# Performance work log

Measured on AMD Instinct MI355X. Metric: run time of the kernel, lower is better.

Reference implementation:

```python
import jax, jax.numpy as jnp
import numpy as np

B, S, D = 2, 2048, 1024
H = 16
HD = D // H  # 64

def setup_inputs() -> dict:
    key = jax.random.key(0)
    ks = jax.random.split(key, 6)
    scale = 0.02
    x   = jax.random.normal(ks[0], (B, S, D), dtype=jnp.float32)
    Wq  = jax.random.normal(ks[1], (D, D), dtype=jnp.float32) * scale
    Wk  = jax.random.normal(ks[2], (D, D), dtype=jnp.float32) * scale
    Wv  = jax.random.normal(ks[3], (D, D), dtype=jnp.float32) * scale
    Wo  = jax.random.normal(ks[4], (D, D), dtype=jnp.float32) * scale
    bo  = jax.random.normal(ks[5], (D,), dtype=jnp.float32) * scale
    return {"x": x, "Wq": Wq, "Wk": Wk, "Wv": Wv, "Wo": Wo, "bo": bo}

def reference(x, Wq, Wk, Wv, Wo, bo):
    b, s, d = x.shape
    # QKV projections (no bias, qkv_bias=False); weights stored as [d_in, d_out]
    q = (x @ Wq).reshape(b, s, H, HD).transpose(0, 2, 1, 3)  # [b,h,s,hd]
    k = (x @ Wk).reshape(b, s, H, HD).transpose(0, 2, 1, 3)
    v = (x @ Wv).reshape(b, s, H, HD).transpose(0, 2, 1, 3)
    scores = jnp.einsum('bhqd,bhkd->bhqk', q, k)  # [b,h,s,s]
    causal = jnp.triu(jnp.ones((s, s), dtype=bool), k=1)
    scores = jnp.where(causal, -jnp.inf, scores)
    attn = jax.nn.softmax(scores / jnp.sqrt(jnp.float32(HD)), axis=-1)
    # dropout_rate = 0.0 -> identity
    ctx = jnp.einsum('bhqk,bhkd->bqhd', attn, v).reshape(b, s, d)
    return ctx @ Wo + bo
```

## Files before the change

kernel.cpp:

```cpp
#include <hip/hip_runtime.h>
#include <hip/hip_bf16.h>
#include <math.h>

#define B_ 2
#define S_ 2048
#define D_ 1024
#define H_ 16
#define HD_ 64
#define M_ (B_*S_)

typedef __attribute__((ext_vector_type(8))) short bf16x8;
typedef __attribute__((ext_vector_type(4))) float f32x4;

#define MFMA16(a,b,c) __builtin_amdgcn_mfma_f32_16x16x32_bf16(a,b,c,0,0,0)
#define INFF __builtin_inff()

static __device__ __forceinline__ unsigned short f2bf_bits(float f) {
    unsigned int u = __float_as_uint(f);
    unsigned int r = (u + 0x7fffu + ((u >> 16) & 1u)) >> 16;
    return (unsigned short)r;
}

static __device__ __forceinline__ void gload16(const unsigned short* g, unsigned short* l) {
    __builtin_amdgcn_global_load_lds(
        (const __attribute__((address_space(1))) unsigned int*)(g),
        (__attribute__((address_space(3))) unsigned int*)(l),
        16, 0, 0);
}

#define PH_END4 do { \
    asm volatile("s_waitcnt vmcnt(4)" ::: "memory"); \
    __builtin_amdgcn_sched_barrier(0); \
    __builtin_amdgcn_s_barrier(); \
    __builtin_amdgcn_sched_barrier(0); \
} while (0)
#define PH_END6 do { \
    asm volatile("s_waitcnt vmcnt(6)" ::: "memory"); \
    __builtin_amdgcn_sched_barrier(0); \
    __builtin_amdgcn_s_barrier(); \
    __builtin_amdgcn_sched_barrier(0); \
} while (0)

__global__ __launch_bounds__(256) void convert_x_kernel(
    const float* __restrict__ x, unsigned short* __restrict__ o) {
    size_t i = (size_t)blockIdx.x * 256 + threadIdx.x;
    float4 v = reinterpret_cast<const float4*>(x)[i];
    ushort4 u;
    u.x = f2bf_bits(v.x); u.y = f2bf_bits(v.y);
    u.z = f2bf_bits(v.z); u.w = f2bf_bits(v.w);
    reinterpret_cast<ushort4*>(o)[i] = u;
}

__global__ __launch_bounds__(256) void convw_kernel(
    const float* __restrict__ W0, const float* __restrict__ W1,
    const float* __restrict__ W2, const float* __restrict__ W3,
    unsigned short* __restrict__ OT) {
    __shared__ float t[32][33];
    const float* W = (blockIdx.z == 0) ? W0 : (blockIdx.z == 1) ? W1
                    : (blockIdx.z == 2) ? W2 : W3;
    unsigned short* O = OT + (size_t)blockIdx.z * D_ * D_;
    int tx = threadIdx.x & 31, ty = threadIdx.x >> 5;
    int kb = blockIdx.y * 32, nb = blockIdx.x * 32;
#pragma unroll
    for (int i = 0; i < 4; i++)
        t[ty + 8*i][tx] = W[(size_t)(kb + ty + 8*i) * D_ + nb + tx];
    __syncthreads();
#pragma unroll
    for (int i = 0; i < 4; i++) {
        int n = nb + ty + 8*i, k = kb + tx;
        O[(size_t)n * D_ + k] = f2bf_bits(t[tx][ty + 8*i]);
    }
}

__global__ __launch_bounds__(512, 2) void gemm_qkv256(
    const unsigned short* __restrict__ A,
    const unsigned short* __restrict__ BT,
    unsigned short* __restrict__ outp)
{
    __shared__ union {
        struct { unsigned short A[2][2][8192]; unsigned short B[2][2][8192]; } s;
        unsigned short vt[256][136];
    } sm;
    const int tid = threadIdx.x, lane = tid & 63, wid = tid >> 6;
    const int lrow = lane & 15, lk8 = lane >> 4, orow = lk8 * 4;
    const int wmo = (wid >> 2) * 64;
    const int wno = (wid & 3) * 32;
    const int m0 = blockIdx.x * 256, n0 = blockIdx.y * 256;

    const int srow = lane >> 3, sgr = lane & 7;
    const unsigned sgo = (unsigned)(wid * 8 + srow) * 1024u
                       + (unsigned)((sgr ^ srow) << 3);
    const unsigned short* Ag = A  + (unsigned)m0 * 1024u + sgo;
    const unsigned short* Bg = BT + (unsigned)n0 * 1024u + sgo;
    const int ldsrb = wid * 512;

    const int sw0 = ((lk8 ^ (lrow & 7)) << 3);
    const int sw1 = (((4 | lk8) ^ (lrow & 7)) << 3);
    int ar[4], br[2];
#pragma unroll
    for (int f = 0; f < 4; f++) ar[f] = (wmo + f * 16 + lrow) * 64;
#pragma unroll
    for (int g = 0; g < 2; g++) br[g] = (wno + g * 16 + lrow) * 64;

    f32x4 acc[8][4] = {};
    bf16x8 af[4][2], bf[2][2];

    auto stA = [&](int par, int mh, unsigned k) {
        unsigned short* d = &sm.s.A[par][mh][ldsrb];
        const unsigned short* g = Ag + (unsigned)mh * 131072u + k;
        gload16(g, d);
        gload16(g + 65536u, d + 4096);
    };
    auto stB = [&](int par, int nh, unsigned k) {
        unsigned short* d = &sm.s.B[par][nh][ldsrb];
        const unsigned short* g = Bg + (unsigned)nh * 131072u + k;
        gload16(g, d);
        gload16(g + 65536u, d + 4096);
    };
    auto lda = [&](int par, int qm) {
        const unsigned short* p = &sm.s.A[par][qm][0];
#pragma unroll
        for (int f = 0; f < 4; f++) {
            af[f][0] = *reinterpret_cast<const bf16x8*>(p + ar[f] + sw0);
            af[f][1] = *reinterpret_cast<const bf16x8*>(p + ar[f] + sw1);
        }
    };
    auto ldb = [&](int par, int qn) {
        const unsigned short* p = &sm.s.B[par][qn][0];
#pragma unroll
        for (int g = 0; g < 2; g++) {
            bf[g][0] = *reinterpret_cast<const bf16x8*>(p + br[g] + sw0);
            bf[g][1] = *reinterpret_cast<const bf16x8*>(p + br[g] + sw1);
        }
    };
    auto mma = [&](int qm, int qn) {
        __builtin_amdgcn_s_setprio(1);
#pragma unroll
        for (int f = 0; f < 4; f++)
#pragma unroll
            for (int g = 0; g < 2; g++)
#pragma unroll
                for (int ks = 0; ks < 2; ks++)
                    acc[qm*4+f][qn*2+g] =
                        MFMA16(af[f][ks], bf[g][ks], acc[qm*4+f][qn*2+g]);
        __builtin_amdgcn_s_setprio(0);
    };

    stB(0, 0, 0); stA(0, 0, 0); stB(0, 1, 0); stA(0, 1, 0);
    PH_END4;

#pragma unroll 1
    for (int t = 0; t < 16; t++) {
        const int par = t & 1, pn = par ^ 1;
        const unsigned kn = (t < 15) ? (unsigned)(t + 1) * 64u : 0u;
        lda(par, 0); ldb(par, 0);  stB(pn, 0, kn);  mma(0, 0);  PH_END4;
        ldb(par, 1);               stA(pn, 0, kn);  mma(0, 1);  PH_END4;
        lda(par, 1);               stB(pn, 1, kn);  mma(1, 1);  PH_END6;
        ldb(par, 0);               stA(pn, 1, kn);  mma(1, 0);  PH_END4;
    }

    asm volatile("s_waitcnt vmcnt(0)" ::: "memory");
    __builtin_amdgcn_sched_barrier(0);
    __builtin_amdgcn_s_barrier();

    const int which = n0 >> 10;
    const int nl0 = n0 & 1023;
    const int bq = m0 >> 11;
    unsigned short* obase = outp + (size_t)which * 4194304;

    if (which < 2) {
        const float scale = (which == 0) ? 0.125f : 1.0f;
#pragma unroll
        for (int fi = 0; fi < 8; fi++)
#pragma unroll
            for (int g = 0; g < 4; g++)
#pragma unroll
                for (int r = 0; r < 4; r++) {
                    int m = m0 + (fi >> 2) * 128 + wmo + (fi & 3) * 16 + orow + r;
                    int n = nl0 + (g >> 1) * 128 + wno + (g & 1) * 16 + lrow;
                    int s = m & 2047;
                    obase[(((size_t)(bq * 16 + (n >> 6)) * 2048 + s) << 6) + (n & 63)]
                        = f2bf_bits(acc[fi][g][r] * scale);
                }
    } else {
#pragma unroll
        for (int qm = 0; qm < 2; qm++) {
#pragma unroll
            for (int f = 0; f < 4; f++)
#pragma unroll
                for (int g = 0; g < 4; g++) {
                    const int ml = wmo + f * 16 + orow;
                    const int nc = (g >> 1) * 128 + wno + (g & 1) * 16 + lrow;
                    uint2 w;
                    w.x = (unsigned)f2bf_bits(acc[qm*4+f][g][0])
                        | ((unsigned)f2bf_bits(acc[qm*4+f][g][1]) << 16);
                    w.y = (unsigned)f2bf_bits(acc[qm*4+f][g][2])
                        | ((unsigned)f2bf_bits(acc[qm*4+f][g][3]) << 16);
                    *reinterpret_cast<uint2*>(&sm.vt[nc][ml]) = w;
                }
            __syncthreads();
            {
                const int row = tid >> 1, c0 = (tid & 1) * 64;
                unsigned short* dst = obase +
                    ((size_t)(bq * 1024) + nl0 + row) * 2048 +
                    (m0 & 2047) + qm * 128 + c0;
#pragma unroll
                for (int j = 0; j < 64; j += 8)
                    *reinterpret_cast<bf16x8*>(dst + j) =
                        *reinterpret_cast<const bf16x8*>(&sm.vt[row][c0 + j]);
            }
            __syncthreads();
        }
    }
}

template<int BN, int MODE>
__global__ __launch_bounds__(256) void gemm_gl(
    const unsigned short* __restrict__ A,
    const unsigned short* __restrict__ BT,
    void* __restrict__ outp,
    const float* __restrict__ bias)
{
    constexpr int K = 1024;
    constexpr int NF = (BN == 128) ? 4 : 2;
    __shared__ struct { unsigned short As[128][64]; unsigned short Bs[BN][64]; } sm;
    const int m0 = blockIdx.x * 128;
    const int n0 = blockIdx.y * BN;
    const int tid = threadIdx.x, lane = tid & 63, wid = tid >> 6;
    const int wm = (wid >> 1) * 64;
    const int wn = (wid & 1) * (BN / 2);
    const int lrow = lane & 15, lk8 = lane >> 4, orow = lk8 * 4;
    f32x4 acc[4][NF] = {};

    for (int k0 = 0; k0 < K; k0 += 64) {
#pragma unroll
        for (int i = 0; i < 4; i++) {
            const int rbase = wid * 32 + i * 8;
            const int rl = rbase + (lane >> 3);
            const int sc = ((lane & 7) ^ (rl & 7)) << 3;
            gload16(A + (size_t)(m0 + rl) * K + k0 + sc, &sm.As[rbase][0]);
        }
#pragma unroll
        for (int i = 0; i < BN / 32; i++) {
            const int rbase = wid * (BN / 4) + i * 8;
            const int rl = rbase + (lane >> 3);
            const int sc = ((lane & 7) ^ (rl & 7)) << 3;
            gload16(BT + (size_t)(n0 + rl) * K + k0 + sc, &sm.Bs[rbase][0]);
        }
        __syncthreads();
#pragma unroll
        for (int ks = 0; ks < 2; ks++) {
            bf16x8 af[4], bfr[NF];
#pragma unroll
            for (int f = 0; f < 4; f++) {
                const int row = wm + f * 16 + lrow;
                const int p = (ks * 4 + lk8) ^ (row & 7);
                af[f] = *reinterpret_cast<const bf16x8*>(&sm.As[row][p * 8]);
            }
#pragma unroll
            for (int f = 0; f < NF; f++) {
                const int row = wn + f * 16 + lrow;
                const int p = (ks * 4 + lk8) ^ (row & 7);
                bfr[f] = *reinterpret_cast<const bf16x8*>(&sm.Bs[row][p * 8]);
            }
            __builtin_amdgcn_s_setprio(1);
#pragma unroll
            for (int mf = 0; mf < 4; mf++)
#pragma unroll
                for (int nf = 0; nf < NF; nf++)
                    acc[mf][nf] = MFMA16(af[mf], bfr[nf], acc[mf][nf]);
            __builtin_amdgcn_s_setprio(0);
        }
        __syncthreads();
    }

    float* o = (float*)outp;
#pragma unroll
    for (int mf = 0; mf < 4; mf++)
#pragma unroll
        for (int nf = 0; nf < NF; nf++)
#pragma unroll
            for (int r = 0; r < 4; r++) {
                int m = m0 + wm + mf*16 + orow + r;
                int n = n0 + wn + nf*16 + lrow;
                o[(size_t)m * 1024 + n] = acc[mf][nf][r] + bias[n];
            }
}

__global__ __launch_bounds__(256) void attn_kernel(
    const unsigned short* __restrict__ Q,
    const unsigned short* __restrict__ Kb,
    const unsigned short* __restrict__ VT,
    unsigned short* __restrict__ ctx)
{
    __shared__ unsigned short Ks[2][64][64];
    __shared__ unsigned short Vs[2][64][64];
    __shared__ unsigned short Pl[4][16][72];
    const int fid = blockIdx.x;
    const int xcd = fid & 7, t = fid >> 3;
    const int bh = xcd | ((t & 3) << 3);
    const int qt = 31 - (t >> 2);
    const int lane = threadIdx.x & 63, wid = threadIdx.x >> 6;
    const int lrow = lane & 15, lk8 = lane >> 4, orow = lk8 * 4;
    const unsigned short* Qp = Q  + (size_t)bh * (S_ * 64);
    const unsigned short* Kp = Kb + (size_t)bh * (S_ * 64);
    const unsigned short* Vp = VT + (size_t)bh * (64 * S_);
    const int b = bh >> 4, h = bh & 15;
    const int q0 = qt * 64 + wid * 16;
    const int nb = qt + 1;

    auto stage = [&](int buf, int kv0) {
#pragma unroll
        for (int i = 0; i < 2; i++) {
            const int rbase = wid * 16 + 8 * i;
            const int rl = rbase + (lane >> 3);
            const int sc = (((lane & 7) ^ (rl & 7)) << 3);
            gload16(Kp + (size_t)(kv0 + rl) * 64 + sc, &Ks[buf][rbase][0]);
            gload16(Vp + (size_t)rl * S_ + kv0 + sc, &Vs[buf][rbase][0]);
        }
    };

    stage(0, 0);

    bf16x8 qf[2];
#pragma unroll
    for (int kt = 0; kt < 2; kt++)
        qf[kt] = *reinterpret_cast<const bf16x8*>(
            Qp + (size_t)(q0 + lrow) * 64 + kt*32 + lk8*8);

    f32x4 acc[4] = {};
    float lr = 0.f;

    __syncthreads();

#pragma unroll 1
    for (int kvb = 0; kvb < nb; kvb++) {
        const int cur = kvb & 1;
        if (kvb + 1 < nb) stage(cur ^ 1, (kvb + 1) * 64);

        f32x4 sacc[4] = {};
        __builtin_amdgcn_s_setprio(1);
#pragma unroll
        for (int kt = 0; kt < 2; kt++)
#pragma unroll
            for (int nf = 0; nf < 4; nf++) {
                const int row = nf * 16 + lrow;
                const int g = ((kt << 2) | lk8) ^ (row & 7);
                bf16x8 kf = *reinterpret_cast<const bf16x8*>(&Ks[cur][row][g << 3]);
                sacc[nf] = MFMA16(kf, qf[kt], sacc[nf]);
            }
        __builtin_amdgcn_s_setprio(0);
        if (kvb == qt) {
#pragma unroll
            for (int nf = 0; nf < 4; nf++)
#pragma unroll
                for (int r = 0; r < 4; r++)
                    if (nf*16 + orow + r > wid*16 + lrow) sacc[nf][r] = -INFF;
        }
#pragma unroll
        for (int nf = 0; nf < 4; nf++)
#pragma unroll
            for (int r = 0; r < 4; r++) {
                float p = __expf(sacc[nf][r]);
                sacc[nf][r] = p;
                lr += p;
            }
#pragma unroll
        for (int nf = 0; nf < 4; nf++) {
            uint2 w;
            w.x = (unsigned)f2bf_bits(sacc[nf][0]) | ((unsigned)f2bf_bits(sacc[nf][1]) << 16);
            w.y = (unsigned)f2bf_bits(sacc[nf][2]) | ((unsigned)f2bf_bits(sacc[nf][3]) << 16);
            *reinterpret_cast<uint2*>(&Pl[wid][lrow][nf*16 + orow]) = w;
        }
        bf16x8 pf[2];
#pragma unroll
        for (int kt = 0; kt < 2; kt++)
            pf[kt] = *reinterpret_cast<const bf16x8*>(&Pl[wid][lrow][kt*32 + lk8*8]);
        __builtin_amdgcn_s_setprio(1);
#pragma unroll
        for (int kt = 0; kt < 2; kt++)
#pragma unroll
            for (int nf = 0; nf < 4; nf++) {
                const int row = nf * 16 + lrow;
                const int g = ((kt << 2) | lk8) ^ (row & 7);
                bf16x8 vf = *reinterpret_cast<const bf16x8*>(&Vs[cur][row][g << 3]);
                acc[nf] = MFMA16(pf[kt], vf, acc[nf]);
            }
        __builtin_amdgcn_s_setprio(0);
        __syncthreads();
    }

    lr += __shfl_xor(lr, 16);
    lr += __shfl_xor(lr, 32);
    const float inv = 1.0f / lr;
#pragma unroll
    for (int r = 0; r < 4; r++) {
        const float linv = __shfl(inv, (lane & 48) + orow + r);
#pragma unroll
        for (int nf = 0; nf < 4; nf++) {
            int s = q0 + orow + r;
            int col = h * 64 + nf * 16 + lrow;
            ctx[((size_t)(b * S_ + s)) * D_ + col] = f2bf_bits(acc[nf][r] * linv);
        }
    }
}

extern "C" void kernel_launch(void* const* d_in, const int* in_sizes, int n_in,
                              void* d_out, int out_size, void* d_ws, size_t ws_size,
                              hipStream_t stream) {
    const float* x  = (const float*)d_in[0];
    const float* Wq = (const float*)d_in[1];
    const float* Wk = (const float*)d_in[2];
    const float* Wv = (const float*)d_in[3];
    const float* Wo = (const float*)d_in[4];
    const float* bo = (const float*)d_in[5];
    float* out = (float*)d_out;

    char* ws = (char*)d_ws;
    unsigned short* xb  = (unsigned short*)(ws);
    unsigned short* WT  = (unsigned short*)(ws + 8388608);
    unsigned short* QKV = (unsigned short*)(ws + 16777216);
    unsigned short* ctx = (unsigned short*)(ws + 41943040);

    unsigned short* Qb  = QKV;
    unsigned short* Kb  = QKV + 4194304;
    unsigned short* VTb = QKV + 8388608;

    convert_x_kernel<<<dim3(4096), dim3(256), 0, stream>>>(x, xb);
    convw_kernel<<<dim3(32, 32, 4), dim3(256), 0, stream>>>(Wq, Wk, Wv, Wo, WT);

    gemm_qkv256<<<dim3(16, 12), dim3(512), 0, stream>>>(xb, WT, QKV);

    attn_kernel<<<dim3(1024), dim3(256), 0, stream>>>(Qb, Kb, VTb, ctx);

    gemm_gl<64, 1><<<dim3(32, 16), dim3(256), 0, stream>>>(
        ctx, WT + 3145728, (void*)out, bo);
}
```

Measured before the change: 106.0 us.

## Issue all GEMM stage loads up front, use exp2 with folded log2e, packed bf16 converts

Result: faster. 102.0 us (-3.8%).

```diff
diff --git a/kernel.cpp b/kernel.cpp
--- a/kernel.cpp
+++ b/kernel.cpp
@@ -14,11 +14,19 @@
 
 #define MFMA16(a,b,c) __builtin_amdgcn_mfma_f32_16x16x32_bf16(a,b,c,0,0,0)
 #define INFF __builtin_inff()
+#define LOG2E 1.44269504088896340736f
+#define EXP2F(x) __builtin_amdgcn_exp2f(x)
 
 static __device__ __forceinline__ unsigned short f2bf_bits(float f) {
     unsigned int u = __float_as_uint(f);
     unsigned int r = (u + 0x7fffu + ((u >> 16) & 1u)) >> 16;
     return (unsigned short)r;
+}
+
+static __device__ __forceinline__ unsigned cvt_pk_bf16(float a, float b) {
+    unsigned r;
+    asm("v_cvt_pk_bf16_f32 %0, %1, %2" : "=v"(r) : "v"(a), "v"(b));
+    return r;
 }
 
 static __device__ __forceinline__ void gload16(const unsigned short* g, unsigned short* l) {
@@ -28,14 +36,13 @@
         16, 0, 0);
 }
 
-#define PH_END4 do { \
-    asm volatile("s_waitcnt vmcnt(4)" ::: "memory"); \
+#define PH_WAIT_BAR(N) do { \
+    asm volatile("s_waitcnt vmcnt(" #N ")" ::: "memory"); \
     __builtin_amdgcn_sched_barrier(0); \
     __builtin_amdgcn_s_barrier(); \
     __builtin_amdgcn_sched_barrier(0); \
 } while (0)
-#define PH_END6 do { \
-    asm volatile("s_waitcnt vmcnt(6)" ::: "memory"); \
+#define PH_BAR do { \
     __builtin_amdgcn_sched_barrier(0); \
     __builtin_amdgcn_s_barrier(); \
     __builtin_amdgcn_sched_barrier(0); \
@@ -147,16 +154,18 @@
     };
 
     stB(0, 0, 0); stA(0, 0, 0); stB(0, 1, 0); stA(0, 1, 0);
-    PH_END4;
+    PH_WAIT_BAR(4);
 
 #pragma unroll 1
     for (int t = 0; t < 16; t++) {
         const int par = t & 1, pn = par ^ 1;
         const unsigned kn = (t < 15) ? (unsigned)(t + 1) * 64u : 0u;
-        lda(par, 0); ldb(par, 0);  stB(pn, 0, kn);  mma(0, 0);  PH_END4;
-        ldb(par, 1);               stA(pn, 0, kn);  mma(0, 1);  PH_END4;
-        lda(par, 1);               stB(pn, 1, kn);  mma(1, 1);  PH_END6;
-        ldb(par, 0);               stA(pn, 1, kn);  mma(1, 0);  PH_END4;
+        lda(par, 0); ldb(par, 0);
+        stB(pn, 0, kn); stA(pn, 0, kn); stB(pn, 1, kn); stA(pn, 1, kn);
+        mma(0, 0);  PH_WAIT_BAR(10);
+        ldb(par, 1);  mma(0, 1);  PH_WAIT_BAR(8);
+        lda(par, 1);  mma(1, 1);  PH_BAR;
+        ldb(par, 0);  mma(1, 0);  PH_WAIT_BAR(4);
     }
 
     asm volatile("s_waitcnt vmcnt(0)" ::: "memory");
@@ -169,7 +178,7 @@
     unsigned short* obase = outp + (size_t)which * 4194304;
 
     if (which < 2) {
-        const float scale = (which == 0) ? 0.125f : 1.0f;
+        const float scale = (which == 0) ? (0.125f * LOG2E) : 1.0f;
 #pragma unroll
         for (int fi = 0; fi < 8; fi++)
 #pragma unroll
@@ -192,10 +201,8 @@
                     const int ml = wmo + f * 16 + orow;
                     const int nc = (g >> 1) * 128 + wno + (g & 1) * 16 + lrow;
                     uint2 w;
-                    w.x = (unsigned)f2bf_bits(acc[qm*4+f][g][0])
-                        | ((unsigned)f2bf_bits(acc[qm*4+f][g][1]) << 16);
-                    w.y = (unsigned)f2bf_bits(acc[qm*4+f][g][2])
-                        | ((unsigned)f2bf_bits(acc[qm*4+f][g][3]) << 16);
+                    w.x = cvt_pk_bf16(acc[qm*4+f][g][0], acc[qm*4+f][g][1]);
+                    w.y = cvt_pk_bf16(acc[qm*4+f][g][2], acc[qm*4+f][g][3]);
                     *reinterpret_cast<uint2*>(&sm.vt[nc][ml]) = w;
                 }
             __syncthreads();
@@ -287,7 +294,7 @@
             }
 }
 
-__global__ __launch_bounds__(256) void attn_kernel(
+__global__ __launch_bounds__(256, 4) void attn_kernel(
     const unsigned short* __restrict__ Q,
     const unsigned short* __restrict__ Kb,
     const unsigned short* __restrict__ VT,
@@ -295,7 +302,7 @@
 {
     __shared__ unsigned short Ks[2][64][64];
     __shared__ unsigned short Vs[2][64][64];
-    __shared__ unsigned short Pl[4][16][72];
+    __shared__ unsigned short Pl[4][16][64];
     const int fid = blockIdx.x;
     const int xcd = fid & 7, t = fid >> 3;
     const int bh = xcd | ((t & 3) << 3);
@@ -308,6 +315,7 @@
     const int b = bh >> 4, h = bh & 15;
     const int q0 = qt * 64 + wid * 16;
     const int nb = qt + 1;
+    const int psw = (lrow & 7) << 3;
 
     auto stage = [&](int buf, int kv0) {
 #pragma unroll
@@ -357,25 +365,27 @@
                 for (int r = 0; r < 4; r++)
                     if (nf*16 + orow + r > wid*16 + lrow) sacc[nf][r] = -INFF;
         }
-#pragma unroll
-        for (int nf = 0; nf < 4; nf++)
-#pragma unroll
-            for (int r = 0; r < 4; r++) {
-                float p = __expf(sacc[nf][r]);
-                sacc[nf][r] = p;
-                lr += p;
-            }
+        float ps[4];
+#pragma unroll
+        for (int nf = 0; nf < 4; nf++) {
+#pragma unroll
+            for (int r = 0; r < 4; r++)
+                sacc[nf][r] = EXP2F(sacc[nf][r]);
+            ps[nf] = (sacc[nf][0] + sacc[nf][1]) + (sacc[nf][2] + sacc[nf][3]);
+        }
+        lr += (ps[0] + ps[1]) + (ps[2] + ps[3]);
 #pragma unroll
         for (int nf = 0; nf < 4; nf++) {
             uint2 w;
-            w.x = (unsigned)f2bf_bits(sacc[nf][0]) | ((unsigned)f2bf_bits(sacc[nf][1]) << 16);
-            w.y = (unsigned)f2bf_bits(sacc[nf][2]) | ((unsigned)f2bf_bits(sacc[nf][3]) << 16);
-            *reinterpret_cast<uint2*>(&Pl[wid][lrow][nf*16 + orow]) = w;
+            w.x = cvt_pk_bf16(sacc[nf][0], sacc[nf][1]);
+            w.y = cvt_pk_bf16(sacc[nf][2], sacc[nf][3]);
+            *reinterpret_cast<uint2*>(&Pl[wid][lrow][(nf*16 + orow) ^ psw]) = w;
         }
         bf16x8 pf[2];
 #pragma unroll
         for (int kt = 0; kt < 2; kt++)
-            pf[kt] = *reinterpret_cast<const bf16x8*>(&Pl[wid][lrow][kt*32 + lk8*8]);
+            pf[kt] = *reinterpret_cast<const bf16x8*>(
+                &Pl[wid][lrow][(kt*32 + lk8*8) ^ psw]);
         __builtin_amdgcn_s_setprio(1);
 #pragma unroll
         for (int kt = 0; kt < 2; kt++)
```
